# Optimization experiments

Hardware: AMD Instinct MI355X
Metric: run time of the kernel (lower is better)

## Reference

```python
import jax, jax.numpy as jnp
import numpy as np

GRID_MIN, GRID_MAX, NUM_GRIDS = -2.0, 2.0, 15
DENOM = (GRID_MAX - GRID_MIN) / (NUM_GRIDS - 1)
LN_EPS = 1e-3  # tf.keras LayerNormalization default epsilon


def setup_inputs() -> dict:
    key = jax.random.key(0)
    k_x, k_sw, k_bw = jax.random.split(key, 3)
    N, D = 32768, 512
    G = NUM_GRIDS
    x = jax.random.normal(k_x, (N, D), dtype=jnp.float32)
    ln_gamma = jnp.ones((D,), dtype=jnp.float32)
    ln_beta = jnp.zeros((D,), dtype=jnp.float32)
    # Glorot-ish scaling to keep outputs sane
    spline_w = jax.random.normal(k_sw, (D, D * G), dtype=jnp.float32) * (1.0 / np.sqrt(D * G))
    base_w = jax.random.normal(k_bw, (D, D), dtype=jnp.float32) * (1.0 / np.sqrt(D))
    base_b = jnp.zeros((D,), dtype=jnp.float32)
    return {"x": x, "ln_gamma": ln_gamma, "ln_beta": ln_beta,
            "spline_w": spline_w, "base_w": base_w, "base_b": base_b}


def reference(x, ln_gamma, ln_beta, spline_w, base_w, base_b):
    N, D = x.shape
    G = NUM_GRIDS
    grid = jnp.linspace(GRID_MIN, GRID_MAX, G).astype(x.dtype)  # non-trainable buffer
    # LayerNorm over last axis (Keras: eps=1e-3)
    mean = jnp.mean(x, axis=-1, keepdims=True)
    var = jnp.mean(jnp.square(x - mean), axis=-1, keepdims=True)
    xn = (x - mean) * jax.lax.rsqrt(var + LN_EPS) * ln_gamma + ln_beta
    # RBF expansion: [N, D, G]
    basis = jnp.exp(-jnp.square((xn[..., None] - grid) / DENOM))
    # Spline GEMM: weight (out, D*G), y = basis_flat @ W^T
    w3 = spline_w.reshape(D, D, G)  # (out, in, grid)
    ret = jnp.einsum('ndg,odg->no', basis, w3)
    # Base residual: Dense(relu(x))
    base = jax.nn.relu(x) @ base_w + base_b
    return ret + base
```

## Files before the change

### kernel.cpp

```cpp
#include <hip/hip_runtime.h>
#include <hip/hip_bf16.h>
#include <stdint.h>

typedef __attribute__((ext_vector_type(8))) short short8;
typedef __attribute__((ext_vector_type(4))) float f32x4;
typedef __attribute__((ext_vector_type(4))) unsigned int u32x4;

#define NROWS 32768
#define DIM 512
#define KTOT 8192
#define KSPL 7680
#define LNEPS 1e-3f
#define SQL 4.20392843f

#if __has_builtin(__builtin_amdgcn_exp2f)
#define EXP2F(x) __builtin_amdgcn_exp2f(x)
#else
#define EXP2F(x) exp2f(x)
#endif

__device__ __forceinline__ unsigned short f2bf(float f) {
    unsigned u = __float_as_uint(f);
    u += 0x7fffu + ((u >> 16) & 1u);
    return (unsigned short)(u >> 16);
}

__device__ __forceinline__ unsigned pack_bf2(float a, float b) {
    unsigned ua = __float_as_uint(a) + 0x8000u;
    unsigned ub = __float_as_uint(b) + 0x8000u;
    return __builtin_amdgcn_perm(ub, ua, 0x07060302u);
}

__global__ __launch_bounds__(256) void prep_w_k(const float* __restrict__ sw,
                                                const float* __restrict__ bwt,
                                                unsigned short* __restrict__ Bw) {
    __shared__ float lds[KSPL];
    const int o = blockIdx.x;
    const int t = threadIdx.x;
    const float* swr = sw + (size_t)o * KSPL;
    unsigned short* br = Bw + (size_t)o * KTOT;
    #pragma unroll
    for (int it = 0; it < 30; ++it) lds[it * 256 + t] = swr[it * 256 + t];
    #pragma unroll
    for (int it = 0; it < 2; ++it) {
        int d = it * 256 + t;
        br[KSPL + d] = f2bf(bwt[(size_t)d * DIM + o]);
    }
    __syncthreads();
    #pragma unroll
    for (int it = 0; it < 30; ++it) {
        int k = it * 256 + t;
        int g = k >> 9, d = k & 511;
        br[k] = f2bf(lds[d * 15 + g]);
    }
}

__global__ __launch_bounds__(1024, 4) void kan_gemm(
    const float* __restrict__ x,
    const unsigned short* __restrict__ Bw,
    const float* __restrict__ gam,
    const float* __restrict__ bet,
    const float* __restrict__ bb,
    float* __restrict__ out) {
    __shared__ __align__(16) short As[128 * 64];
    __shared__ __align__(16) short Bs[512 * 64];

    const int t = threadIdx.x;
    const int w = t >> 6, l = t & 63;
    const int n0 = blockIdx.x << 7;

    const int ar  = t >> 3;
    const int kkg = t & 7;
    const int wm = (w >> 3) << 6;
    const int wn = (w & 7) << 6;
    const int fm = l & 15, fq = l >> 4;
    const int brow = l >> 3;
    const int bxor = (l & 7) ^ brow;
    const int asto = ((ar << 3) | (kkg ^ (ar & 7))) << 3;

    const float* xrow = x + (size_t)(n0 + ar) * DIM;
    float s = 0.f, ss = 0.f;
    #pragma unroll
    for (int it = 0; it < 16; ++it) {
        float4 v = *(const float4*)(xrow + it * 32 + ((t & 7) << 2));
        s  += v.x + v.y + v.z + v.w;
        ss += v.x * v.x + v.y * v.y + v.z * v.z + v.w * v.w;
    }
    #pragma unroll
    for (int m = 4; m >= 1; m >>= 1) {
        s  += __shfl_xor(s,  m, 64);
        ss += __shfl_xor(ss, m, 64);
    }
    const float mean = s * (1.0f / DIM);
    const float rstd = rsqrtf(ss * (1.0f / DIM) - mean * mean + LNEPS);
    const float sr = SQL * rstd;

    f32x4 acc[4][4];
    #pragma unroll
    for (int i = 0; i < 4; ++i)
        #pragma unroll
        for (int j = 0; j < 4; ++j)
            acc[i][j] = (f32x4)0.0f;

    #pragma unroll 1
    for (int dsb = 0; dsb < 8; ++dsb) {
        const int d0 = dsb << 6;
        const int dc = d0 + (kkg << 3);
        float xr[8], q[8];
        {
            float4 a = *(const float4*)(xrow + dc);
            float4 b = *(const float4*)(xrow + dc + 4);
            xr[0] = a.x; xr[1] = a.y; xr[2] = a.z; xr[3] = a.w;
            xr[4] = b.x; xr[5] = b.y; xr[6] = b.z; xr[7] = b.w;
            float4 g0 = *(const float4*)(gam + dc);
            float4 g1 = *(const float4*)(gam + dc + 4);
            float4 b0 = *(const float4*)(bet + dc);
            float4 b1 = *(const float4*)(bet + dc + 4);
            float gv[8] = {g0.x, g0.y, g0.z, g0.w, g1.x, g1.y, g1.z, g1.w};
            float bv[8] = {b0.x, b0.y, b0.z, b0.w, b1.x, b1.y, b1.z, b1.w};
            #pragma unroll
            for (int j = 0; j < 8; ++j) {
                float c = sr * gv[j];
                float o = __builtin_fmaf(-mean, c, SQL * bv[j]);
                q[j] = __builtin_fmaf(xr[j], c, o);
            }
        }
        #pragma unroll 1
        for (int g = 0; g < 16; ++g) {
            const int kc = (g < 15) ? ((g << 9) + d0) : (KSPL + d0);
            #pragma unroll
            for (int i = 0; i < 4; ++i) {
                const int rb = (i << 7) + (w << 3);
                const unsigned short* gp =
                    Bw + (size_t)(rb + brow) * KTOT + kc + (bxor << 3);
                __builtin_amdgcn_global_load_lds(
                    (const __attribute__((address_space(1))) void*)gp,
                    (__attribute__((address_space(3))) void*)&Bs[rb << 6],
                    16, 0, 0);
            }
            u32x4 v;
            if (g < 15) {
                const float qg = SQL * (-2.0f + (float)g * (2.0f / 7.0f));
                float e[8];
                #pragma unroll
                for (int j = 0; j < 8; ++j) {
                    float d = q[j] - qg;
                    e[j] = EXP2F(-(d * d));
                }
                v[0] = pack_bf2(e[0], e[1]);
                v[1] = pack_bf2(e[2], e[3]);
                v[2] = pack_bf2(e[4], e[5]);
                v[3] = pack_bf2(e[6], e[7]);
            } else {
                v[0] = pack_bf2(fmaxf(xr[0], 0.f), fmaxf(xr[1], 0.f));
                v[1] = pack_bf2(fmaxf(xr[2], 0.f), fmaxf(xr[3], 0.f));
                v[2] = pack_bf2(fmaxf(xr[4], 0.f), fmaxf(xr[5], 0.f));
                v[3] = pack_bf2(fmaxf(xr[6], 0.f), fmaxf(xr[7], 0.f));
            }
            *(u32x4*)&As[asto] = v;
            __syncthreads();
            #pragma unroll
            for (int ks = 0; ks < 2; ++ks) {
                const int kg = (ks << 2) + fq;
                short8 af[4], bfr[4];
                #pragma unroll
                for (int mt = 0; mt < 4; ++mt) {
                    const int m = wm + (mt << 4) + fm;
                    af[mt] = *(const short8*)&As[((m << 3) | (kg ^ (m & 7))) << 3];
                }
                #pragma unroll
                for (int nt = 0; nt < 4; ++nt) {
                    const int n = wn + (nt << 4) + fm;
                    bfr[nt] = *(const short8*)&Bs[((n << 3) | (kg ^ (n & 7))) << 3];
                }
                #pragma unroll
                for (int mt = 0; mt < 4; ++mt)
                    #pragma unroll
                    for (int nt = 0; nt < 4; ++nt)
                        acc[mt][nt] = __builtin_amdgcn_mfma_f32_16x16x32_bf16(
                            af[mt], bfr[nt], acc[mt][nt], 0, 0, 0);
            }
            __syncthreads();
        }
    }
    const int rq = fq << 2;
    float bias[4];
    #pragma unroll
    for (int nt = 0; nt < 4; ++nt) bias[nt] = bb[wn + (nt << 4) + fm];
    #pragma unroll
    for (int mt = 0; mt < 4; ++mt) {
        #pragma unroll
        for (int nt = 0; nt < 4; ++nt) {
            const int gr = n0 + wm + (mt << 4) + rq;
            const int gc = wn + (nt << 4) + fm;
            #pragma unroll
            for (int r = 0; r < 4; ++r)
                out[(size_t)(gr + r) * DIM + gc] = acc[mt][nt][r] + bias[nt];
        }
    }
}

extern "C" void kernel_launch(void* const* d_in, const int* in_sizes, int n_in,
                              void* d_out, int out_size, void* d_ws, size_t ws_size,
                              hipStream_t stream) {
    const float* x   = (const float*)d_in[0];
    const float* gam = (const float*)d_in[1];
    const float* bet = (const float*)d_in[2];
    const float* sw  = (const float*)d_in[3];
    const float* bwt = (const float*)d_in[4];
    const float* bb  = (const float*)d_in[5];
    float* out = (float*)d_out;

    unsigned short* Bw = (unsigned short*)d_ws;

    prep_w_k<<<dim3(512), dim3(256), 0, stream>>>(sw, bwt, Bw);
    kan_gemm<<<dim3(256), dim3(1024), 0, stream>>>(x, Bw, gam, bet, bb, out);
}
```

Measured before the change: 392.5 us.

## Double-buffer LDS tiles to overlap B prefetch and basis computation with MFMA

After: 591.0 us. 1.51x slower.

```diff
diff --git a/kernel.cpp b/kernel.cpp
--- a/kernel.cpp
+++ b/kernel.cpp
@@ -62,8 +62,8 @@
     const float* __restrict__ bet,
     const float* __restrict__ bb,
     float* __restrict__ out) {
-    __shared__ __align__(16) short As[128 * 64];
-    __shared__ __align__(16) short Bs[512 * 64];
+    __shared__ __align__(16) short As[2][128 * 64];
+    __shared__ __align__(16) short Bs[2][512 * 64];
 
     const int t = threadIdx.x;
     const int w = t >> 6, l = t & 63;
@@ -102,87 +102,115 @@
         for (int j = 0; j < 4; ++j)
             acc[i][j] = (f32x4)0.0f;
 
+    float xr[8], q[8];
+
+    auto loadq = [&](int dn) {
+        const int dc = (dn << 6) + (kkg << 3);
+        float4 a = *(const float4*)(xrow + dc);
+        float4 b = *(const float4*)(xrow + dc + 4);
+        xr[0] = a.x; xr[1] = a.y; xr[2] = a.z; xr[3] = a.w;
+        xr[4] = b.x; xr[5] = b.y; xr[6] = b.z; xr[7] = b.w;
+        float4 g0 = *(const float4*)(gam + dc);
+        float4 g1 = *(const float4*)(gam + dc + 4);
+        float4 b0 = *(const float4*)(bet + dc);
+        float4 b1 = *(const float4*)(bet + dc + 4);
+        float gv[8] = {g0.x, g0.y, g0.z, g0.w, g1.x, g1.y, g1.z, g1.w};
+        float bv[8] = {b0.x, b0.y, b0.z, b0.w, b1.x, b1.y, b1.z, b1.w};
+        #pragma unroll
+        for (int j = 0; j < 8; ++j) {
+            float c = sr * gv[j];
+            float o = __builtin_fmaf(-mean, c, SQL * bv[j]);
+            q[j] = __builtin_fmaf(xr[j], c, o);
+        }
+    };
+
+    auto stageB = [&](int nb, int kc) {
+        #pragma unroll
+        for (int i = 0; i < 4; ++i) {
+            const int rb = (i << 7) + (w << 3);
+            const unsigned short* gp =
+                Bw + (size_t)(rb + brow) * KTOT + kc + (bxor << 3);
+            __builtin_amdgcn_global_load_lds(
+                (const __attribute__((address_space(1))) void*)gp,
+                (__attribute__((address_space(3))) void*)&Bs[nb][rb << 6],
+                16, 0, 0);
+        }
+    };
+
+    auto stageA = [&](int nb, int gn) {
+        u32x4 v;
+        if (gn < 15) {
+            const float qg = SQL * (-2.0f + (float)gn * (2.0f / 7.0f));
+            float e[8];
+            #pragma unroll
+            for (int j = 0; j < 8; ++j) {
+                float d = q[j] - qg;
+                e[j] = EXP2F(-(d * d));
+            }
+            v[0] = pack_bf2(e[0], e[1]);
+            v[1] = pack_bf2(e[2], e[3]);
+            v[2] = pack_bf2(e[4], e[5]);
+            v[3] = pack_bf2(e[6], e[7]);
+        } else {
+            v[0] = pack_bf2(fmaxf(xr[0], 0.f), fmaxf(xr[1], 0.f));
+            v[1] = pack_bf2(fmaxf(xr[2], 0.f), fmaxf(xr[3], 0.f));
+            v[2] = pack_bf2(fmaxf(xr[4], 0.f), fmaxf(xr[5], 0.f));
+            v[3] = pack_bf2(fmaxf(xr[6], 0.f), fmaxf(xr[7], 0.f));
+        }
+        *(u32x4*)&As[nb][asto] = v;
+    };
+
+    loadq(0);
+    stageB(0, 0);
+    stageA(0, 0);
+    asm volatile("s_waitcnt vmcnt(0) lgkmcnt(0)" ::: "memory");
+    __builtin_amdgcn_s_barrier();
+
+    auto do_step = [&](int sidx, int cur) {
+        const int nb = cur ^ 1;
+        const int nxt = sidx + 1;
+        const bool more = (nxt < 128);
+        if (more) {
+            const int gn = nxt & 15, dn = nxt >> 4, d0n = dn << 6;
+            stageB(nb, (gn < 15) ? ((gn << 9) + d0n) : (KSPL + d0n));
+            if (gn == 0) loadq(dn);
+        }
+        const short* Asc = As[cur];
+        const short* Bsc = Bs[cur];
+        __builtin_amdgcn_s_setprio(1);
+        #pragma unroll
+        for (int ks = 0; ks < 2; ++ks) {
+            const int kg = (ks << 2) + fq;
+            short8 af[4], bfr[4];
+            #pragma unroll
+            for (int mt = 0; mt < 4; ++mt) {
+                const int m = wm + (mt << 4) + fm;
+                af[mt] = *(const short8*)&Asc[((m << 3) | (kg ^ (m & 7))) << 3];
+            }
+            #pragma unroll
+            for (int nt = 0; nt < 4; ++nt) {
+                const int n = wn + (nt << 4) + fm;
+                bfr[nt] = *(const short8*)&Bsc[((n << 3) | (kg ^ (n & 7))) << 3];
+            }
+            #pragma unroll
+            for (int mt = 0; mt < 4; ++mt)
+                #pragma unroll
+                for (int nt = 0; nt < 4; ++nt)
+                    acc[mt][nt] = __builtin_amdgcn_mfma_f32_16x16x32_bf16(
+                        af[mt], bfr[nt], acc[mt][nt], 0, 0, 0);
+        }
+        __builtin_amdgcn_s_setprio(0);
+        if (more) stageA(nb, nxt & 15);
+        asm volatile("s_waitcnt vmcnt(0) lgkmcnt(0)" ::: "memory");
+        __builtin_amdgcn_s_barrier();
+    };
+
     #pragma unroll 1
-    for (int dsb = 0; dsb < 8; ++dsb) {
-        const int d0 = dsb << 6;
-        const int dc = d0 + (kkg << 3);
-        float xr[8], q[8];
-        {
-            float4 a = *(const float4*)(xrow + dc);
-            float4 b = *(const float4*)(xrow + dc + 4);
-            xr[0] = a.x; xr[1] = a.y; xr[2] = a.z; xr[3] = a.w;
-            xr[4] = b.x; xr[5] = b.y; xr[6] = b.z; xr[7] = b.w;
-            float4 g0 = *(const float4*)(gam + dc);
-            float4 g1 = *(const float4*)(gam + dc + 4);
-            float4 b0 = *(const float4*)(bet + dc);
-            float4 b1 = *(const float4*)(bet + dc + 4);
-            float gv[8] = {g0.x, g0.y, g0.z, g0.w, g1.x, g1.y, g1.z, g1.w};
-            float bv[8] = {b0.x, b0.y, b0.z, b0.w, b1.x, b1.y, b1.z, b1.w};
-            #pragma unroll
-            for (int j = 0; j < 8; ++j) {
-                float c = sr * gv[j];
-                float o = __builtin_fmaf(-mean, c, SQL * bv[j]);
-                q[j] = __builtin_fmaf(xr[j], c, o);
-            }
-        }
-        #pragma unroll 1
-        for (int g = 0; g < 16; ++g) {
-            const int kc = (g < 15) ? ((g << 9) + d0) : (KSPL + d0);
-            #pragma unroll
-            for (int i = 0; i < 4; ++i) {
-                const int rb = (i << 7) + (w << 3);
-                const unsigned short* gp =
-                    Bw + (size_t)(rb + brow) * KTOT + kc + (bxor << 3);
-                __builtin_amdgcn_global_load_lds(
-                    (const __attribute__((address_space(1))) void*)gp,
-                    (__attribute__((address_space(3))) void*)&Bs[rb << 6],
-                    16, 0, 0);
-            }
-            u32x4 v;
-            if (g < 15) {
-                const float qg = SQL * (-2.0f + (float)g * (2.0f / 7.0f));
-                float e[8];
-                #pragma unroll
-                for (int j = 0; j < 8; ++j) {
-                    float d = q[j] - qg;
-                    e[j] = EXP2F(-(d * d));
-                }
-                v[0] = pack_bf2(e[0], e[1]);
-                v[1] = pack_bf2(e[2], e[3]);
-                v[2] = pack_bf2(e[4], e[5]);
-                v[3] = pack_bf2(e[6], e[7]);
-            } else {
-                v[0] = pack_bf2(fmaxf(xr[0], 0.f), fmaxf(xr[1], 0.f));
-                v[1] = pack_bf2(fmaxf(xr[2], 0.f), fmaxf(xr[3], 0.f));
-                v[2] = pack_bf2(fmaxf(xr[4], 0.f), fmaxf(xr[5], 0.f));
-                v[3] = pack_bf2(fmaxf(xr[6], 0.f), fmaxf(xr[7], 0.f));
-            }
-            *(u32x4*)&As[asto] = v;
-            __syncthreads();
-            #pragma unroll
-            for (int ks = 0; ks < 2; ++ks) {
-                const int kg = (ks << 2) + fq;
-                short8 af[4], bfr[4];
-                #pragma unroll
-                for (int mt = 0; mt < 4; ++mt) {
-                    const int m = wm + (mt << 4) + fm;
-                    af[mt] = *(const short8*)&As[((m << 3) | (kg ^ (m & 7))) << 3];
-                }
-                #pragma unroll
-                for (int nt = 0; nt < 4; ++nt) {
-                    const int n = wn + (nt << 4) + fm;
-                    bfr[nt] = *(const short8*)&Bs[((n << 3) | (kg ^ (n & 7))) << 3];
-                }
-                #pragma unroll
-                for (int mt = 0; mt < 4; ++mt)
-                    #pragma unroll
-                    for (int nt = 0; nt < 4; ++nt)
-                        acc[mt][nt] = __builtin_amdgcn_mfma_f32_16x16x32_bf16(
-                            af[mt], bfr[nt], acc[mt][nt], 0, 0, 0);
-            }
-            __syncthreads();
-        }
-    }
+    for (int sp = 0; sp < 64; ++sp) {
+        do_step(2 * sp, 0);
+        do_step(2 * sp + 1, 1);
+    }
+
     const int rq = fq << 2;
     float bias[4];
     #pragma unroll
```

## Double-buffer A tile, read B directly from global, single barrier per step

Applied to the files above, without the earlier changes.

Result: slower. 654.6 us (+66.8%).

```diff
diff --git a/kernel.cpp b/kernel.cpp
--- a/kernel.cpp
+++ b/kernel.cpp
@@ -62,8 +62,7 @@
     const float* __restrict__ bet,
     const float* __restrict__ bb,
     float* __restrict__ out) {
-    __shared__ __align__(16) short As[128 * 64];
-    __shared__ __align__(16) short Bs[512 * 64];
+    __shared__ __align__(16) short As[2][128 * 64];
 
     const int t = threadIdx.x;
     const int w = t >> 6, l = t & 63;
@@ -74,9 +73,12 @@
     const int wm = (w >> 3) << 6;
     const int wn = (w & 7) << 6;
     const int fm = l & 15, fq = l >> 4;
-    const int brow = l >> 3;
-    const int bxor = (l & 7) ^ brow;
     const int asto = ((ar << 3) | (kkg ^ (ar & 7))) << 3;
+
+    int voffB[4];
+    #pragma unroll
+    for (int nt = 0; nt < 4; ++nt)
+        voffB[nt] = (wn + (nt << 4) + fm) * KTOT + (fq << 3);
 
     const float* xrow = x + (size_t)(n0 + ar) * DIM;
     float s = 0.f, ss = 0.f;
@@ -102,87 +104,93 @@
         for (int j = 0; j < 4; ++j)
             acc[i][j] = (f32x4)0.0f;
 
-    #pragma unroll 1
-    for (int dsb = 0; dsb < 8; ++dsb) {
-        const int d0 = dsb << 6;
-        const int dc = d0 + (kkg << 3);
-        float xr[8], q[8];
-        {
+    float q[8];
+
+    auto loadq = [&](int dn) {
+        const int dc = (dn << 6) + (kkg << 3);
+        float4 a = *(const float4*)(xrow + dc);
+        float4 b = *(const float4*)(xrow + dc + 4);
+        float xv[8] = {a.x, a.y, a.z, a.w, b.x, b.y, b.z, b.w};
+        float4 g0 = *(const float4*)(gam + dc);
+        float4 g1 = *(const float4*)(gam + dc + 4);
+        float4 b0 = *(const float4*)(bet + dc);
+        float4 b1 = *(const float4*)(bet + dc + 4);
+        float gv[8] = {g0.x, g0.y, g0.z, g0.w, g1.x, g1.y, g1.z, g1.w};
+        float bv[8] = {b0.x, b0.y, b0.z, b0.w, b1.x, b1.y, b1.z, b1.w};
+        #pragma unroll
+        for (int j = 0; j < 8; ++j) {
+            float c = sr * gv[j];
+            float o = __builtin_fmaf(-mean, c, SQL * bv[j]);
+            q[j] = __builtin_fmaf(xv[j], c, o);
+        }
+    };
+
+    auto stageA = [&](int nb, int gp, int dn) {
+        u32x4 v;
+        if (gp < 15) {
+            const float qg = SQL * (-2.0f + (float)gp * (2.0f / 7.0f));
+            float e[8];
+            #pragma unroll
+            for (int j = 0; j < 8; ++j) {
+                float d = q[j] - qg;
+                e[j] = EXP2F(-(d * d));
+            }
+            v[0] = pack_bf2(e[0], e[1]);
+            v[1] = pack_bf2(e[2], e[3]);
+            v[2] = pack_bf2(e[4], e[5]);
+            v[3] = pack_bf2(e[6], e[7]);
+        } else {
+            const int dc = (dn << 6) + (kkg << 3);
             float4 a = *(const float4*)(xrow + dc);
             float4 b = *(const float4*)(xrow + dc + 4);
-            xr[0] = a.x; xr[1] = a.y; xr[2] = a.z; xr[3] = a.w;
-            xr[4] = b.x; xr[5] = b.y; xr[6] = b.z; xr[7] = b.w;
-            float4 g0 = *(const float4*)(gam + dc);
-            float4 g1 = *(const float4*)(gam + dc + 4);
-            float4 b0 = *(const float4*)(bet + dc);
-            float4 b1 = *(const float4*)(bet + dc + 4);
-            float gv[8] = {g0.x, g0.y, g0.z, g0.w, g1.x, g1.y, g1.z, g1.w};
-            float bv[8] = {b0.x, b0.y, b0.z, b0.w, b1.x, b1.y, b1.z, b1.w};
-            #pragma unroll
-            for (int j = 0; j < 8; ++j) {
-                float c = sr * gv[j];
-                float o = __builtin_fmaf(-mean, c, SQL * bv[j]);
-                q[j] = __builtin_fmaf(xr[j], c, o);
+            v[0] = pack_bf2(fmaxf(a.x, 0.f), fmaxf(a.y, 0.f));
+            v[1] = pack_bf2(fmaxf(a.z, 0.f), fmaxf(a.w, 0.f));
+            v[2] = pack_bf2(fmaxf(b.x, 0.f), fmaxf(b.y, 0.f));
+            v[3] = pack_bf2(fmaxf(b.z, 0.f), fmaxf(b.w, 0.f));
+        }
+        *(u32x4*)&As[nb][asto] = v;
+    };
+
+    loadq(0);
+    stageA(0, 0, 0);
+    __syncthreads();
+
+    #pragma unroll 1
+    for (int sp = 0; sp < 128; ++sp) {
+        const int c = sp & 1;
+        const int g = sp & 15, dsb = sp >> 4;
+        const int kc = (g < 15) ? ((g << 9) + (dsb << 6)) : (KSPL + (dsb << 6));
+        const int snx = sp + 1;
+        if (snx < 128) {
+            const int g1 = snx & 15, d1 = snx >> 4;
+            if (g1 == 0) loadq(d1);
+            stageA(c ^ 1, g1, d1);
+        }
+        const unsigned short* bbase = Bw + kc;
+        const short* Asc = &As[c][0];
+        #pragma unroll
+        for (int ks = 0; ks < 2; ++ks) {
+            short8 bfr[4];
+            #pragma unroll
+            for (int nt = 0; nt < 4; ++nt)
+                bfr[nt] = *(const short8*)(bbase + voffB[nt] + (ks << 5));
+            const int kg = (ks << 2) + fq;
+            short8 af[4];
+            #pragma unroll
+            for (int mt = 0; mt < 4; ++mt) {
+                const int m = wm + (mt << 4) + fm;
+                af[mt] = *(const short8*)&Asc[((m << 3) | (kg ^ (m & 7))) << 3];
             }
-        }
-        #pragma unroll 1
-        for (int g = 0; g < 16; ++g) {
-            const int kc = (g < 15) ? ((g << 9) + d0) : (KSPL + d0);
-            #pragma unroll
-            for (int i = 0; i < 4; ++i) {
-                const int rb = (i << 7) + (w << 3);
-                const unsigned short* gp =
-                    Bw + (size_t)(rb + brow) * KTOT + kc + (bxor << 3);
-                __builtin_amdgcn_global_load_lds(
-                    (const __attribute__((address_space(1))) void*)gp,
-                    (__attribute__((address_space(3))) void*)&Bs[rb << 6],
-                    16, 0, 0);
-            }
-            u32x4 v;
-            if (g < 15) {
-                const float qg = SQL * (-2.0f + (float)g * (2.0f / 7.0f));
-                float e[8];
+            #pragma unroll
+            for (int mt = 0; mt < 4; ++mt)
                 #pragma unroll
-                for (int j = 0; j < 8; ++j) {
-                    float d = q[j] - qg;
-                    e[j] = EXP2F(-(d * d));
-                }
-                v[0] = pack_bf2(e[0], e[1]);
-                v[1] = pack_bf2(e[2], e[3]);
-                v[2] = pack_bf2(e[4], e[5]);
-                v[3] = pack_bf2(e[6], e[7]);
-            } else {
-                v[0] = pack_bf2(fmaxf(xr[0], 0.f), fmaxf(xr[1], 0.f));
-                v[1] = pack_bf2(fmaxf(xr[2], 0.f), fmaxf(xr[3], 0.f));
-                v[2] = pack_bf2(fmaxf(xr[4], 0.f), fmaxf(xr[5], 0.f));
-                v[3] = pack_bf2(fmaxf(xr[6], 0.f), fmaxf(xr[7], 0.f));
-            }
-            *(u32x4*)&As[asto] = v;
-            __syncthreads();
-            #pragma unroll
-            for (int ks = 0; ks < 2; ++ks) {
-                const int kg = (ks << 2) + fq;
-                short8 af[4], bfr[4];
-                #pragma unroll
-                for (int mt = 0; mt < 4; ++mt) {
-                    const int m = wm + (mt << 4) + fm;
-                    af[mt] = *(const short8*)&As[((m << 3) | (kg ^ (m & 7))) << 3];
-                }
-                #pragma unroll
-                for (int nt = 0; nt < 4; ++nt) {
-                    const int n = wn + (nt << 4) + fm;
-                    bfr[nt] = *(const short8*)&Bs[((n << 3) | (kg ^ (n & 7))) << 3];
-                }
-                #pragma unroll
-                for (int mt = 0; mt < 4; ++mt)
-                    #pragma unroll
-                    for (int nt = 0; nt < 4; ++nt)
-                        acc[mt][nt] = __builtin_amdgcn_mfma_f32_16x16x32_bf16(
-                            af[mt], bfr[nt], acc[mt][nt], 0, 0, 0);
-            }
-            __syncthreads();
-        }
-    }
+                for (int nt = 0; nt < 4; ++nt)
+                    acc[mt][nt] = __builtin_amdgcn_mfma_f32_16x16x32_bf16(
+                        af[mt], bfr[nt], acc[mt][nt], 0, 0, 0);
+        }
+        __syncthreads();
+    }
+
     const int rq = fq << 2;
     float bias[4];
     #pragma unroll
```

## Double K-tile depth per iteration and reorder weight layout into contiguous blocks

Applied to the files above, without the earlier changes.

New measurement: 584.1 us. 48.8% more time.

```diff
diff --git a/kernel.cpp b/kernel.cpp
--- a/kernel.cpp
+++ b/kernel.cpp
@@ -34,7 +34,7 @@
 __global__ __launch_bounds__(256) void prep_w_k(const float* __restrict__ sw,
                                                 const float* __restrict__ bwt,
                                                 unsigned short* __restrict__ Bw) {
-    __shared__ float lds[KSPL];
+    __shared__ float lds[KTOT];
     const int o = blockIdx.x;
     const int t = threadIdx.x;
     const float* swr = sw + (size_t)o * KSPL;
@@ -44,14 +44,17 @@
     #pragma unroll
     for (int it = 0; it < 2; ++it) {
         int d = it * 256 + t;
-        br[KSPL + d] = f2bf(bwt[(size_t)d * DIM + o]);
+        lds[KSPL + d] = bwt[(size_t)d * DIM + o];
     }
     __syncthreads();
     #pragma unroll
-    for (int it = 0; it < 30; ++it) {
+    for (int it = 0; it < 32; ++it) {
         int k = it * 256 + t;
-        int g = k >> 9, d = k & 511;
-        br[k] = f2bf(lds[d * 15 + g]);
+        int dsb = k >> 10, r = k & 1023;
+        int j = r >> 7, glo = (r >> 6) & 1, dlo = r & 63;
+        int g = 2 * j + glo, d = (dsb << 6) + dlo;
+        float v = (g < 15) ? lds[d * 15 + g] : lds[KSPL + d];
+        br[k] = f2bf(v);
     }
 }
 
@@ -62,8 +65,8 @@
     const float* __restrict__ bet,
     const float* __restrict__ bb,
     float* __restrict__ out) {
-    __shared__ __align__(16) short As[128 * 64];
-    __shared__ __align__(16) short Bs[512 * 64];
+    __shared__ __align__(16) short As[128 * 128];
+    __shared__ __align__(16) short Bs[512 * 128];
 
     const int t = threadIdx.x;
     const int w = t >> 6, l = t & 63;
@@ -74,9 +77,9 @@
     const int wm = (w >> 3) << 6;
     const int wn = (w & 7) << 6;
     const int fm = l & 15, fq = l >> 4;
-    const int brow = l >> 3;
-    const int bxor = (l & 7) ^ brow;
-    const int asto = ((ar << 3) | (kkg ^ (ar & 7))) << 3;
+    const int brow4 = l >> 4;
+    const int g16 = l & 15;
+    const int sgA = kkg ^ (ar & 7);
 
     const float* xrow = x + (size_t)(n0 + ar) * DIM;
     float s = 0.f, ss = 0.f;
@@ -126,52 +129,73 @@
             }
         }
         #pragma unroll 1
-        for (int g = 0; g < 16; ++g) {
-            const int kc = (g < 15) ? ((g << 9) + d0) : (KSPL + d0);
-            #pragma unroll
-            for (int i = 0; i < 4; ++i) {
-                const int rb = (i << 7) + (w << 3);
+        for (int j = 0; j < 8; ++j) {
+            const int kc = (dsb << 10) + (j << 7);
+            #pragma unroll
+            for (int i = 0; i < 8; ++i) {
+                const int rb = (w << 5) + (i << 2);
+                const int row = rb + brow4;
+                const int srcg = (g16 & 8) | ((g16 ^ (row & 7)) & 7);
                 const unsigned short* gp =
-                    Bw + (size_t)(rb + brow) * KTOT + kc + (bxor << 3);
+                    Bw + (size_t)row * KTOT + kc + (srcg << 3);
                 __builtin_amdgcn_global_load_lds(
                     (const __attribute__((address_space(1))) void*)gp,
-                    (__attribute__((address_space(3))) void*)&Bs[rb << 6],
+                    (__attribute__((address_space(3))) void*)&Bs[rb << 7],
                     16, 0, 0);
             }
-            u32x4 v;
-            if (g < 15) {
-                const float qg = SQL * (-2.0f + (float)g * (2.0f / 7.0f));
+            {
+                const float qg0 = SQL * (-2.0f + (float)(2 * j) * (2.0f / 7.0f));
                 float e[8];
                 #pragma unroll
-                for (int j = 0; j < 8; ++j) {
-                    float d = q[j] - qg;
-                    e[j] = EXP2F(-(d * d));
-                }
+                for (int jj = 0; jj < 8; ++jj) {
+                    float d = q[jj] - qg0;
+                    e[jj] = EXP2F(-(d * d));
+                }
+                u32x4 v;
                 v[0] = pack_bf2(e[0], e[1]);
                 v[1] = pack_bf2(e[2], e[3]);
                 v[2] = pack_bf2(e[4], e[5]);
                 v[3] = pack_bf2(e[6], e[7]);
-            } else {
-                v[0] = pack_bf2(fmaxf(xr[0], 0.f), fmaxf(xr[1], 0.f));
-                v[1] = pack_bf2(fmaxf(xr[2], 0.f), fmaxf(xr[3], 0.f));
-                v[2] = pack_bf2(fmaxf(xr[4], 0.f), fmaxf(xr[5], 0.f));
-                v[3] = pack_bf2(fmaxf(xr[6], 0.f), fmaxf(xr[7], 0.f));
-            }
-            *(u32x4*)&As[asto] = v;
+                *(u32x4*)&As[(ar << 7) + (sgA << 3)] = v;
+            }
+            {
+                u32x4 v;
+                if (j < 7) {
+                    const float qg1 = SQL * (-2.0f + (float)(2 * j + 1) * (2.0f / 7.0f));
+                    float e[8];
+                    #pragma unroll
+                    for (int jj = 0; jj < 8; ++jj) {
+                        float d = q[jj] - qg1;
+                        e[jj] = EXP2F(-(d * d));
+                    }
+                    v[0] = pack_bf2(e[0], e[1]);
+                    v[1] = pack_bf2(e[2], e[3]);
+                    v[2] = pack_bf2(e[4], e[5]);
+                    v[3] = pack_bf2(e[6], e[7]);
+                } else {
+                    v[0] = pack_bf2(fmaxf(xr[0], 0.f), fmaxf(xr[1], 0.f));
+                    v[1] = pack_bf2(fmaxf(xr[2], 0.f), fmaxf(xr[3], 0.f));
+                    v[2] = pack_bf2(fmaxf(xr[4], 0.f), fmaxf(xr[5], 0.f));
+                    v[3] = pack_bf2(fmaxf(xr[6], 0.f), fmaxf(xr[7], 0.f));
+                }
+                *(u32x4*)&As[(ar << 7) + 64 + (sgA << 3)] = v;
+            }
             __syncthreads();
             #pragma unroll
-            for (int ks = 0; ks < 2; ++ks) {
+            for (int ks = 0; ks < 4; ++ks) {
                 const int kg = (ks << 2) + fq;
                 short8 af[4], bfr[4];
                 #pragma unroll
                 for (int mt = 0; mt < 4; ++mt) {
                     const int m = wm + (mt << 4) + fm;
-                    af[mt] = *(const short8*)&As[((m << 3) | (kg ^ (m & 7))) << 3];
+                    const int gA = (kg & 8) | ((kg ^ (m & 7)) & 7);
+                    af[mt] = *(const short8*)&As[(m << 7) + (gA << 3)];
                 }
                 #pragma unroll
                 for (int nt = 0; nt < 4; ++nt) {
                     const int n = wn + (nt << 4) + fm;
-                    bfr[nt] = *(const short8*)&Bs[((n << 3) | (kg ^ (n & 7))) << 3];
+                    const int gB = (kg & 8) | ((kg ^ (n & 7)) & 7);
+                    bfr[nt] = *(const short8*)&Bs[(n << 7) + (gB << 3)];
                 }
                 #pragma unroll
                 for (int mt = 0; mt < 4; ++mt)
```
